# Kernel optimization log

Measured on AMD Instinct MI355X. Metric: run time of the kernel, lower is better.

## Reference

```python
import jax, jax.numpy as jnp
import numpy as np

DIM = 512
HEADS = 8
HEAD_DIM = DIM // HEADS
FF = 2048
WIN = 128
TIME_DIM = 512
B, N = 8, 8192
EPS = 1e-5
NEG = -1e9


def setup_inputs() -> dict:
    key = jax.random.key(0)
    ks = jax.random.split(key, 16)
    def lin(k, fan_in, fan_out):
        bound = 1.0 / np.sqrt(fan_in)
        kw, kb = jax.random.split(k)
        W = jax.random.uniform(kw, (fan_in, fan_out), jnp.float32, -bound, bound)
        b = jax.random.uniform(kb, (fan_out,), jnp.float32, -bound, bound)
        return W, b
    qkv_w, qkv_b = lin(ks[0], DIM, 3 * DIM)
    proj_w, proj_b = lin(ks[1], DIM, DIM)
    mlp_w1, mlp_b1 = lin(ks[2], DIM, FF)
    mlp_w2, mlp_b2 = lin(ks[3], FF, DIM)
    time_w, time_b = lin(ks[4], TIME_DIM, 2 * DIM)
    return {
        "x": jax.random.normal(ks[5], (B, N, DIM), jnp.float32),
        "t_emb": jax.random.normal(ks[6], (B, TIME_DIM), jnp.float32),
        "ln1_g": jnp.ones((DIM,), jnp.float32), "ln1_b": jnp.zeros((DIM,), jnp.float32),
        "qkv_w": qkv_w, "qkv_b": qkv_b,
        "proj_w": proj_w, "proj_b": proj_b,
        "ln2_g": jnp.ones((DIM,), jnp.float32), "ln2_b": jnp.zeros((DIM,), jnp.float32),
        "mlp_w1": mlp_w1, "mlp_b1": mlp_b1,
        "mlp_w2": mlp_w2, "mlp_b2": mlp_b2,
        "time_w": time_w, "time_b": time_b,
    }


def _layernorm(x, g, b):
    mu = jnp.mean(x, -1, keepdims=True)
    var = jnp.mean(jnp.square(x - mu), -1, keepdims=True)
    return (x - mu) * jax.lax.rsqrt(var + EPS) * g + b


def _local_attention(q, k, v, w):
    # q,k,v: [B, h, N, d]; each w-window attends to [prev|cur|next] windows.
    Bh_B, h, n, d = q.shape
    nW = n // w
    qw = q.reshape(Bh_B * h, nW, w, d)
    kw = k.reshape(Bh_B * h, nW, w, d)
    vw = v.reshape(Bh_B * h, nW, w, d)
    pad = lambda t: jnp.pad(t, ((0, 0), (1, 1), (0, 0), (0, 0)))
    kp, vp = pad(kw), pad(vw)
    # context: [Bh, nW, 3w, d]
    kc = jnp.concatenate([kp[:, :-2], kp[:, 1:-1], kp[:, 2:]], axis=2)
    vc = jnp.concatenate([vp[:, :-2], vp[:, 1:-1], vp[:, 2:]], axis=2)
    wv = jnp.pad(jnp.ones((nW,), bool), (1, 1))  # window validity
    valid = jnp.concatenate([
        jnp.repeat(wv[:-2, None], w, 1),
        jnp.repeat(wv[1:-1, None], w, 1),
        jnp.repeat(wv[2:, None], w, 1)], axis=1)  # [nW, 3w]
    sim = jnp.einsum('bnid,bnjd->bnij', qw, kc) * (d ** -0.5)
    sim = jnp.where(valid[None, :, None, :], sim, NEG)
    attn = jax.nn.softmax(sim, axis=-1)
    out = jnp.einsum('bnij,bnjd->bnid', attn, vc)
    return out.reshape(Bh_B, h, n, d)


def reference(x, t_emb, ln1_g, ln1_b, qkv_w, qkv_b, proj_w, proj_b,
              ln2_g, ln2_b, mlp_w1, mlp_b1, mlp_w2, mlp_b2, time_w, time_b):
    Bq, n, c = x.shape
    ss = jax.nn.silu(t_emb) @ time_w + time_b  # [B, 2C]
    scale, shift = ss[:, :c], ss[:, c:]
    x_norm = _layernorm(x, ln1_g, ln1_b) * (1.0 + scale[:, None, :]) + shift[:, None, :]
    qkv = (x_norm @ qkv_w + qkv_b).reshape(Bq, n, 3, HEADS, HEAD_DIM)
    qkv = jnp.transpose(qkv, (2, 0, 3, 1, 4))  # [3, B, h, N, d]
    q, k, v = qkv[0], qkv[1], qkv[2]
    attn_out = _local_attention(q, k, v, WIN)  # [B, h, N, d]
    attn_out = jnp.transpose(attn_out, (0, 2, 1, 3)).reshape(Bq, n, c)
    x = x + (attn_out @ proj_w + proj_b)
    h2 = _layernorm(x, ln2_g, ln2_b)
    mlp = jax.nn.gelu(h2 @ mlp_w1 + mlp_b1, approximate=False) @ mlp_w2 + mlp_b2
    return x + mlp
```

## Files before the change

### kernel.cpp

```cpp
#include <hip/hip_runtime.h>
#include <cstdint>
#include <cstddef>

#define DIM   512
#define HEADS 8
#define HD    64
#define FF    2048
#define WINSZ 128
#define BB    8
#define NN    8192
#define NW    (NN / WINSZ)
#define MROWS (BB * NN)
#define QS    ((size_t)BB * HEADS * NN * HD)

typedef __attribute__((ext_vector_type(8))) _Float16 half8;
typedef __attribute__((ext_vector_type(4))) float floatx4;

__device__ __forceinline__ floatx4 mfma16(half8 a, half8 b, floatx4 c) {
    return __builtin_amdgcn_mfma_f32_16x16x32_f16(a, b, c, 0, 0, 0);
}

__device__ __forceinline__ void gload_lds16(const void* g, void* l) {
    __builtin_amdgcn_global_load_lds(
        (const __attribute__((address_space(1))) void*)g,
        (__attribute__((address_space(3))) void*)l, 16, 0, 0);
}

__device__ __forceinline__ float qmax16(float v) {
    v = fmaxf(v, __shfl_xor(v, 1));
    v = fmaxf(v, __shfl_xor(v, 2));
    v = fmaxf(v, __shfl_xor(v, 4));
    v = fmaxf(v, __shfl_xor(v, 8));
    return v;
}
__device__ __forceinline__ float qsum16(float v) {
    v += __shfl_xor(v, 1);
    v += __shfl_xor(v, 2);
    v += __shfl_xor(v, 4);
    v += __shfl_xor(v, 8);
    return v;
}

__device__ __forceinline__ float gelu_f(float x) {
    const float y = 1.5957691216f * (x + 0.044715f * x * x * x);
    const float t = 1.0f - 2.0f / (__expf(y) + 1.0f);
    return 0.5f * x * (1.0f + t);
}

__global__ __launch_bounds__(128)
void time_ss_kernel(const float* __restrict__ t_emb, const float* __restrict__ tw,
                    const float* __restrict__ tb, float* __restrict__ ss) {
    __shared__ float st[512];
    const int b = blockIdx.x;
    for (int i = threadIdx.x; i < 512; i += 128) {
        float v = t_emb[b * 512 + i];
        st[i] = v / (1.0f + expf(-v));
    }
    __syncthreads();
    const int j = blockIdx.y * 128 + threadIdx.x;
    float acc = tb[j];
    for (int i = 0; i < 512; ++i) acc += st[i] * tw[i * 1024 + j];
    ss[b * 1024 + j] = acc;
}

__global__ __launch_bounds__(256)
void wcast_kernel(const float* __restrict__ w, _Float16* __restrict__ wt, int K, int N) {
    __shared__ float t[32][33];
    const int kb = blockIdx.x * 32, nb = blockIdx.y * 32;
    const int tx = threadIdx.x & 31, ty = threadIdx.x >> 5;
#pragma unroll
    for (int i = 0; i < 32; i += 8)
        t[ty + i][tx] = w[(size_t)(kb + ty + i) * N + nb + tx];
    __syncthreads();
#pragma unroll
    for (int i = 0; i < 32; i += 8)
        wt[(size_t)(nb + ty + i) * K + kb + tx] = (_Float16)t[tx][ty + i];
}

__global__ __launch_bounds__(256)
void ln_kernel(const float* __restrict__ x, const float* __restrict__ g,
               const float* __restrict__ bv, const float* __restrict__ ss,
               _Float16* __restrict__ out) {
    const int row  = blockIdx.x * 4 + (threadIdx.x >> 6);
    const int lane = threadIdx.x & 63;
    const float* xr = x + (size_t)row * DIM;
    const float4 v0 = *(const float4*)(xr + lane * 4);
    const float4 v1 = *(const float4*)(xr + 256 + lane * 4);
    float s  = v0.x + v0.y + v0.z + v0.w + v1.x + v1.y + v1.z + v1.w;
    float s2 = v0.x * v0.x + v0.y * v0.y + v0.z * v0.z + v0.w * v0.w +
               v1.x * v1.x + v1.y * v1.y + v1.z * v1.z + v1.w * v1.w;
#pragma unroll
    for (int m = 1; m < 64; m <<= 1) {
        s  += __shfl_xor(s, m);
        s2 += __shfl_xor(s2, m);
    }
    const float mean = s * (1.0f / 512.0f);
    const float var  = s2 * (1.0f / 512.0f) - mean * mean;
    const float rstd = rsqrtf(var + 1e-5f);
    const int b = row >> 13;
    const float vv[8] = {v0.x, v0.y, v0.z, v0.w, v1.x, v1.y, v1.z, v1.w};
    union { _Float16 h[4]; unsigned long long u; } pk;
#pragma unroll
    for (int half = 0; half < 2; ++half) {
        const int c0 = half * 256 + lane * 4;
#pragma unroll
        for (int i = 0; i < 4; ++i) {
            const int c = c0 + i;
            float y = (vv[half * 4 + i] - mean) * rstd * g[c] + bv[c];
            y = y * (1.0f + ss[b * 1024 + c]) + ss[b * 1024 + 512 + c];
            pk.h[i] = (_Float16)y;
        }
        *(unsigned long long*)(out + (size_t)row * DIM + c0) = pk.u;
    }
}

__global__ __launch_bounds__(256)
void ln_h_kernel(const _Float16* __restrict__ x, const float* __restrict__ g,
                 const float* __restrict__ bv, _Float16* __restrict__ out) {
    const int row  = blockIdx.x * 4 + (threadIdx.x >> 6);
    const int lane = threadIdx.x & 63;
    half8 v = *(const half8*)(x + (size_t)row * DIM + lane * 8);
    float f[8];
    float s = 0.f, s2 = 0.f;
#pragma unroll
    for (int i = 0; i < 8; ++i) {
        f[i] = (float)v[i];
        s += f[i];
        s2 += f[i] * f[i];
    }
#pragma unroll
    for (int m = 1; m < 64; m <<= 1) {
        s  += __shfl_xor(s, m);
        s2 += __shfl_xor(s2, m);
    }
    const float mean = s * (1.0f / 512.0f);
    const float var  = s2 * (1.0f / 512.0f) - mean * mean;
    const float rstd = rsqrtf(var + 1e-5f);
    half8 o;
#pragma unroll
    for (int i = 0; i < 8; ++i) {
        const int c = lane * 8 + i;
        o[i] = (_Float16)((f[i] - mean) * rstd * g[c] + bv[c]);
    }
    *(half8*)(out + (size_t)row * DIM + lane * 8) = o;
}

template <int EPI>
__global__ __launch_bounds__(256)
void gemm_bt(const _Float16* __restrict__ A, const _Float16* __restrict__ BT,
             const float* __restrict__ bias, int K, int N,
             const float* __restrict__ residf, const _Float16* __restrict__ residh,
             float* __restrict__ outf, _Float16* __restrict__ outh) {
    __shared__ _Float16 lA[128 * 64];
    __shared__ _Float16 lB[128 * 64];
    const int tid  = threadIdx.x;
    const int wv   = tid >> 6;
    const int lane = tid & 63;
    const int ln   = lane & 15;
    const int qd   = lane >> 4;
    const int wm   = (wv >> 1) * 64;
    const int wn   = (wv & 1) * 64;

    const int nbx = gridDim.x;
    const int l   = blockIdx.y * nbx + blockIdx.x;
    const int grp = l / (nbx * 8);
    const int rem = l - grp * (nbx * 8);
    const int m0  = (grp * 8 + (rem & 7)) * 128;
    const int n0  = (rem >> 3) * 128;

    floatx4 acc[4][4];
#pragma unroll
    for (int i = 0; i < 4; ++i)
#pragma unroll
        for (int j = 0; j < 4; ++j) acc[i][j] = (floatx4){0.f, 0.f, 0.f, 0.f};

    for (int kt = 0; kt < K; kt += 64) {
        __syncthreads();
#pragma unroll
        for (int i = 0; i < 4; ++i) {
            const int c   = tid + i * 256;
            const int row = c >> 3;
            const int src = ((c & 7) ^ (row & 7)) * 8;
            const int base = (wv * 64 + i * 256) * 8;
            gload_lds16(A + (size_t)(m0 + row) * K + kt + src, &lA[base]);
            gload_lds16(BT + (size_t)(n0 + row) * K + kt + src, &lB[base]);
        }
        __syncthreads();
#pragma unroll
        for (int ks = 0; ks < 2; ++ks) {
            half8 af[4], bf[4];
#pragma unroll
            for (int mi = 0; mi < 4; ++mi) {
                const int row = wm + mi * 16 + ln;
                af[mi] = *(const half8*)&lA[row * 64 + (((ks * 4 + qd) ^ (row & 7)) << 3)];
            }
#pragma unroll
            for (int ni = 0; ni < 4; ++ni) {
                const int row = wn + ni * 16 + ln;
                bf[ni] = *(const half8*)&lB[row * 64 + (((ks * 4 + qd) ^ (row & 7)) << 3)];
            }
#pragma unroll
            for (int mi = 0; mi < 4; ++mi)
#pragma unroll
                for (int ni = 0; ni < 4; ++ni)
                    acc[mi][ni] = mfma16(af[mi], bf[ni], acc[mi][ni]);
        }
    }

#pragma unroll
    for (int mi = 0; mi < 4; ++mi) {
#pragma unroll
        for (int ni = 0; ni < 4; ++ni) {
            const int col  = n0 + wn + ni * 16 + ln;
            const float bb = bias[col];
#pragma unroll
            for (int r = 0; r < 4; ++r) {
                const int row = m0 + wm + mi * 16 + qd * 4 + r;
                const float v = acc[mi][ni][r] + bb;
                if (EPI == 0) {
                    const int which = col >> 9, cc = col & 511;
                    const int b = row >> 13, t = row & 8191;
                    const int h = cc >> 6, d = cc & 63;
                    outh[(size_t)which * QS +
                         ((size_t)(b * HEADS + h) * NN + t) * HD + d] = (_Float16)v;
                } else if (EPI == 1) {
                    const size_t idx = (size_t)row * N + col;
                    outh[idx] = (_Float16)(residf[idx] + v);
                } else if (EPI == 3) {
                    const size_t idx = (size_t)row * N + col;
                    outf[idx] = (float)residh[idx] + v;
                } else {
                    outh[(size_t)row * N + col] = (_Float16)gelu_f(v);
                }
            }
        }
    }
}

__global__ __launch_bounds__(256)
void attn_kernel(const _Float16* __restrict__ qkv, _Float16* __restrict__ attn) {
    const int w  = blockIdx.x;
    const int bh = blockIdx.y;
    const int tid  = threadIdx.x;
    const int wv   = tid >> 6;
    const int lane = tid & 63;
    const int ln   = lane & 15;
    const int qd   = lane >> 4;

    __shared__ _Float16 vt[64 * 136];
    __shared__ _Float16 pl[4 * 32 * 136];

    const _Float16* qbuf = qkv;
    const _Float16* kbuf = qkv + QS;
    const _Float16* vbuf = qkv + 2 * QS;
    const size_t bhbase = (size_t)bh * NN * HD;

    half8 qf[2][2];
    const _Float16* qsrc = qbuf + bhbase + (size_t)(w * WINSZ + wv * 32) * HD;
#pragma unroll
    for (int mt = 0; mt < 2; ++mt)
#pragma unroll
        for (int ks = 0; ks < 2; ++ks)
            qf[mt][ks] = *(const half8*)(qsrc + (mt * 16 + ln) * HD + ks * 32 + qd * 8);

    float mrun[2][4], lrun[2][4];
    floatx4 oacc[2][4];
#pragma unroll
    for (int mt = 0; mt < 2; ++mt)
#pragma unroll
        for (int r = 0; r < 4; ++r) { mrun[mt][r] = -3.0e38f; lrun[mt][r] = 0.f; }
#pragma unroll
    for (int mt = 0; mt < 2; ++mt)
#pragma unroll
        for (int dt = 0; dt < 4; ++dt) oacc[mt][dt] = (floatx4){0.f, 0.f, 0.f, 0.f};

    for (int c = 0; c < 3; ++c) {
        const int kvw = w + c - 1;
        if (kvw < 0 || kvw >= NW) continue;
        __syncthreads();
        const _Float16* vsrc = vbuf + bhbase + (size_t)kvw * WINSZ * HD;
#pragma unroll
        for (int j = 0; j < 4; ++j) {
            const int cc = tid + j * 256;
            const int s = cc >> 3, d0 = (cc & 7) * 8;
            half8 vvv = *(const half8*)(vsrc + cc * 8);
#pragma unroll
            for (int e = 0; e < 8; ++e) vt[(d0 + e) * 136 + s] = vvv[e];
        }
        __syncthreads();

        const _Float16* ksrc = kbuf + bhbase + (size_t)kvw * WINSZ * HD;
        floatx4 sacc[2][8];
#pragma unroll
        for (int nt = 0; nt < 8; ++nt) {
            half8 b0 = *(const half8*)(ksrc + (nt * 16 + ln) * HD + qd * 8);
            half8 b1 = *(const half8*)(ksrc + (nt * 16 + ln) * HD + 32 + qd * 8);
#pragma unroll
            for (int mt = 0; mt < 2; ++mt) {
                floatx4 t = mfma16(qf[mt][0], b0, (floatx4){0.f, 0.f, 0.f, 0.f});
                sacc[mt][nt] = mfma16(qf[mt][1], b1, t);
            }
        }

        _Float16* pw = pl + wv * 32 * 136;
#pragma unroll
        for (int mt = 0; mt < 2; ++mt) {
#pragma unroll
            for (int r = 0; r < 4; ++r) {
                float mx = -3.0e38f;
#pragma unroll
                for (int nt = 0; nt < 8; ++nt)
                    mx = fmaxf(mx, sacc[mt][nt][r] * 0.125f);
                mx = qmax16(mx);
                const float mnew  = fmaxf(mrun[mt][r], mx);
                const float alpha = __expf(mrun[mt][r] - mnew);
                float rs = 0.f;
#pragma unroll
                for (int nt = 0; nt < 8; ++nt) {
                    const float pv = __expf(sacc[mt][nt][r] * 0.125f - mnew);
                    rs += pv;
                    pw[(mt * 16 + qd * 4 + r) * 136 + nt * 16 + ln] = (_Float16)pv;
                }
                rs = qsum16(rs);
                lrun[mt][r] = lrun[mt][r] * alpha + rs;
                mrun[mt][r] = mnew;
#pragma unroll
                for (int dt = 0; dt < 4; ++dt) oacc[mt][dt][r] *= alpha;
            }
        }

#pragma unroll
        for (int kt = 0; kt < 4; ++kt) {
            half8 pf0 = *(const half8*)(pw + ln * 136 + kt * 32 + qd * 8);
            half8 pf1 = *(const half8*)(pw + (16 + ln) * 136 + kt * 32 + qd * 8);
#pragma unroll
            for (int dt = 0; dt < 4; ++dt) {
                half8 vf = *(const half8*)&vt[(dt * 16 + ln) * 136 + kt * 32 + qd * 8];
                oacc[0][dt] = mfma16(pf0, vf, oacc[0][dt]);
                oacc[1][dt] = mfma16(pf1, vf, oacc[1][dt]);
            }
        }
    }

    const int b = bh >> 3, h = bh & 7;
#pragma unroll
    for (int mt = 0; mt < 2; ++mt) {
#pragma unroll
        for (int dt = 0; dt < 4; ++dt) {
#pragma unroll
            for (int r = 0; r < 4; ++r) {
                const int trow = w * WINSZ + wv * 32 + mt * 16 + qd * 4 + r;
                const int col  = h * HD + dt * 16 + ln;
                attn[((size_t)b * NN + trow) * DIM + col] =
                    (_Float16)(oacc[mt][dt][r] / lrun[mt][r]);
            }
        }
    }
}

extern "C" void kernel_launch(void* const* d_in, const int* in_sizes, int n_in,
                              void* d_out, int out_size, void* d_ws, size_t ws_size,
                              hipStream_t stream) {
    const float* x      = (const float*)d_in[0];
    const float* t_emb  = (const float*)d_in[1];
    const float* ln1_g  = (const float*)d_in[2];
    const float* ln1_b  = (const float*)d_in[3];
    const float* qkv_w  = (const float*)d_in[4];
    const float* qkv_b  = (const float*)d_in[5];
    const float* proj_w = (const float*)d_in[6];
    const float* proj_b = (const float*)d_in[7];
    const float* ln2_g  = (const float*)d_in[8];
    const float* ln2_b  = (const float*)d_in[9];
    const float* mlp_w1 = (const float*)d_in[10];
    const float* mlp_b1 = (const float*)d_in[11];
    const float* mlp_w2 = (const float*)d_in[12];
    const float* mlp_b2 = (const float*)d_in[13];
    const float* time_w = (const float*)d_in[14];
    const float* time_b = (const float*)d_in[15];
    float* out = (float*)d_out;

    char* p = (char*)d_ws;
    auto alloc = [&](size_t bytes) {
        char* r = p;
        p += (bytes + 255) & ~(size_t)255;
        return r;
    };
    float*    ss   = (float*)alloc(8 * 1024 * 4);
    _Float16* wq   = (_Float16*)alloc((size_t)1536 * 512 * 2);
    _Float16* wp   = (_Float16*)alloc((size_t)512 * 512 * 2);
    _Float16* w1t  = (_Float16*)alloc((size_t)2048 * 512 * 2);
    _Float16* w2t  = (_Float16*)alloc((size_t)512 * 2048 * 2);
    _Float16* h2   = (_Float16*)alloc((size_t)MROWS * 512 * 2);
    _Float16* x1h  = (_Float16*)alloc((size_t)MROWS * 512 * 2);
    _Float16* regA = (_Float16*)alloc((size_t)MROWS * 512 * 2);
    _Float16* regB = (_Float16*)alloc((size_t)3 * MROWS * 512 * 2);
    _Float16* xn     = regA;
    _Float16* attn   = regA;
    _Float16* qkvb   = regB;
    _Float16* hidden = regA;
    (void)ws_size; (void)in_sizes; (void)n_in; (void)out_size;

    wcast_kernel<<<dim3(512 / 32, 1536 / 32), 256, 0, stream>>>(qkv_w, wq, 512, 1536);
    wcast_kernel<<<dim3(512 / 32, 512 / 32), 256, 0, stream>>>(proj_w, wp, 512, 512);
    wcast_kernel<<<dim3(512 / 32, 2048 / 32), 256, 0, stream>>>(mlp_w1, w1t, 512, 2048);
    wcast_kernel<<<dim3(2048 / 32, 512 / 32), 256, 0, stream>>>(mlp_w2, w2t, 2048, 512);
    time_ss_kernel<<<dim3(8, 8), 128, 0, stream>>>(t_emb, time_w, time_b, ss);
    ln_kernel<<<dim3(MROWS / 4), 256, 0, stream>>>(x, ln1_g, ln1_b, ss, xn);
    gemm_bt<0><<<dim3(1536 / 128, MROWS / 128), 256, 0, stream>>>(
        xn, wq, qkv_b, 512, 1536, nullptr, nullptr, nullptr, qkvb);
    attn_kernel<<<dim3(NW, BB * HEADS), 256, 0, stream>>>(qkvb, attn);
    gemm_bt<1><<<dim3(512 / 128, MROWS / 128), 256, 0, stream>>>(
        attn, wp, proj_b, 512, 512, x, nullptr, nullptr, x1h);
    ln_h_kernel<<<dim3(MROWS / 4), 256, 0, stream>>>(x1h, ln2_g, ln2_b, h2);
    gemm_bt<2><<<dim3(2048 / 128, MROWS / 128), 256, 0, stream>>>(
        h2, w1t, mlp_b1, 512, 2048, nullptr, nullptr, nullptr, hidden);
    gemm_bt<3><<<dim3(512 / 128, MROWS / 128), 256, 0, stream>>>(
        hidden, w2t, mlp_b2, 2048, 512, nullptr, x1h, out, nullptr);
}
```

Before: 1.241 ms.

## Rewrite GEMM as 256x256 double-buffered LDS pipeline with 512 threads

The fp16 MFMA GEMM moves from 128x128 tiles with 256 threads and one synchronised LDS stage to 256x256 tiles with 8 waves. A double-buffered 128KB LDS ring is filled by async global_load_lds prefetches of the next K-halves, interleaved with the MFMA phases under explicit sched/s_barriers and s_setprio. The aim is to hide global-load latency behind compute and raise reuse per LDS byte. The cost is large LDS use, which limits occupancy to one block per CU despite the launch bound of 2. It also adds more accumulator registers and fewer blocks for the narrow N=512 GEMMs.

```diff
diff --git a/kernel.cpp b/kernel.cpp
--- a/kernel.cpp
+++ b/kernel.cpp
@@ -46,6 +46,10 @@
     const float t = 1.0f - 2.0f / (__expf(y) + 1.0f);
     return 0.5f * x * (1.0f + t);
 }
+
+#define SBAR() do { __builtin_amdgcn_sched_barrier(0); \
+                    __builtin_amdgcn_s_barrier();      \
+                    __builtin_amdgcn_sched_barrier(0); } while (0)
 
 __global__ __launch_bounds__(128)
 void time_ss_kernel(const float* __restrict__ t_emb, const float* __restrict__ tw,
@@ -146,77 +150,146 @@
 }
 
 template <int EPI>
-__global__ __launch_bounds__(256)
+__global__ __launch_bounds__(512, 2)
 void gemm_bt(const _Float16* __restrict__ A, const _Float16* __restrict__ BT,
              const float* __restrict__ bias, int K, int N,
              const float* __restrict__ residf, const _Float16* __restrict__ residh,
              float* __restrict__ outf, _Float16* __restrict__ outh) {
-    __shared__ _Float16 lA[128 * 64];
-    __shared__ _Float16 lB[128 * 64];
+    __shared__ __align__(16) _Float16 lds[65536];
     const int tid  = threadIdx.x;
     const int wv   = tid >> 6;
     const int lane = tid & 63;
     const int ln   = lane & 15;
     const int qd   = lane >> 4;
-    const int wm   = (wv >> 1) * 64;
-    const int wn   = (wv & 1) * 64;
+    const int wr   = wv >> 2;
+    const int wc   = wv & 3;
+    const int NT   = K >> 6;
 
     const int nbx = gridDim.x;
     const int l   = blockIdx.y * nbx + blockIdx.x;
     const int grp = l / (nbx * 8);
     const int rem = l - grp * (nbx * 8);
-    const int m0  = (grp * 8 + (rem & 7)) * 128;
-    const int n0  = (rem >> 3) * 128;
-
-    floatx4 acc[4][4];
-#pragma unroll
-    for (int i = 0; i < 4; ++i)
-#pragma unroll
-        for (int j = 0; j < 4; ++j) acc[i][j] = (floatx4){0.f, 0.f, 0.f, 0.f};
-
-    for (int kt = 0; kt < K; kt += 64) {
-        __syncthreads();
-#pragma unroll
-        for (int i = 0; i < 4; ++i) {
-            const int c   = tid + i * 256;
-            const int row = c >> 3;
-            const int src = ((c & 7) ^ (row & 7)) * 8;
-            const int base = (wv * 64 + i * 256) * 8;
-            gload_lds16(A + (size_t)(m0 + row) * K + kt + src, &lA[base]);
-            gload_lds16(BT + (size_t)(n0 + row) * K + kt + src, &lB[base]);
-        }
-        __syncthreads();
-#pragma unroll
-        for (int ks = 0; ks < 2; ++ks) {
-            half8 af[4], bf[4];
-#pragma unroll
-            for (int mi = 0; mi < 4; ++mi) {
-                const int row = wm + mi * 16 + ln;
-                af[mi] = *(const half8*)&lA[row * 64 + (((ks * 4 + qd) ^ (row & 7)) << 3)];
-            }
-#pragma unroll
-            for (int ni = 0; ni < 4; ++ni) {
-                const int row = wn + ni * 16 + ln;
-                bf[ni] = *(const half8*)&lB[row * 64 + (((ks * 4 + qd) ^ (row & 7)) << 3)];
-            }
-#pragma unroll
-            for (int mi = 0; mi < 4; ++mi)
-#pragma unroll
-                for (int ni = 0; ni < 4; ++ni)
-                    acc[mi][ni] = mfma16(af[mi], bf[ni], acc[mi][ni]);
-        }
-    }
-
-#pragma unroll
-    for (int mi = 0; mi < 4; ++mi) {
-#pragma unroll
-        for (int ni = 0; ni < 4; ++ni) {
-            const int col  = n0 + wn + ni * 16 + ln;
-            const float bb = bias[col];
+    const int m0  = (grp * 8 + (rem & 7)) * 256;
+    const int n0  = (rem >> 3) * 256;
+
+    const int c1  = tid + 512;
+    const int sr0 = tid >> 2, sr1 = c1 >> 2;
+    const int so0 = (((tid & 3) ^ (sr0 & 3)) << 3);
+    const int so1 = (((c1 & 3) ^ (sr1 & 3)) << 3);
+    const _Float16* aS0 = A  + (size_t)(m0 + sr0) * K + so0;
+    const _Float16* aS1 = A  + (size_t)(m0 + sr1) * K + so1;
+    const _Float16* bS0 = BT + (size_t)(n0 + sr0) * K + so0;
+    const _Float16* bS1 = BT + (size_t)(n0 + sr1) * K + so1;
+    const int dst0 = (wv * 64) * 8;
+    const int dst1 = (wv * 64 + 512) * 8;
+
+    auto stA = [&](int buf, int kh, int ktEl) {
+        _Float16* r = &lds[buf * 32768 + kh * 8192];
+        gload_lds16(aS0 + ktEl + kh * 32, r + dst0);
+        gload_lds16(aS1 + ktEl + kh * 32, r + dst1);
+    };
+    auto stB = [&](int buf, int kh, int ktEl) {
+        _Float16* r = &lds[buf * 32768 + 16384 + kh * 8192];
+        gload_lds16(bS0 + ktEl + kh * 32, r + dst0);
+        gload_lds16(bS1 + ktEl + kh * 32, r + dst1);
+    };
+
+    int rA[8], rB[4];
+#pragma unroll
+    for (int f = 0; f < 8; ++f) {
+        const int row = wr * 128 + f * 16 + ln;
+        rA[f] = row * 32 + ((qd ^ (row & 3)) << 3);
+    }
+#pragma unroll
+    for (int n = 0; n < 4; ++n) {
+        const int row = wc * 64 + n * 16 + ln;
+        rB[n] = row * 32 + ((qd ^ (row & 3)) << 3);
+    }
+
+    floatx4 acc[8][4];
+#pragma unroll
+    for (int f = 0; f < 8; ++f)
+#pragma unroll
+        for (int n = 0; n < 4; ++n) acc[f][n] = (floatx4){0.f, 0.f, 0.f, 0.f};
+
+    stA(0, 0, 0); stB(0, 0, 0); stA(0, 1, 0); stB(0, 1, 0);
+    stA(1, 0, 64); stB(1, 0, 64);
+    asm volatile("s_waitcnt vmcnt(4)" ::: "memory");
+    SBAR();
+
+    auto do_tile = [&](int t, int buf) {
+        const int ab = buf * 32768;
+        const int bb = buf * 32768 + 16384;
+        const bool s1 = (t + 1 < NT);
+        const bool s2 = (t + 2 < NT);
+        half8 af[4], bf[4];
+#pragma unroll
+        for (int f = 0; f < 4; ++f) af[f] = *(const half8*)&lds[ab + rA[f]];
+#pragma unroll
+        for (int n = 0; n < 4; ++n) bf[n] = *(const half8*)&lds[bb + rB[n]];
+        if (s1) stA(buf ^ 1, 1, (t + 1) * 64);
+        SBAR();
+        __builtin_amdgcn_s_setprio(1);
+#pragma unroll
+        for (int f = 0; f < 4; ++f)
+#pragma unroll
+            for (int n = 0; n < 4; ++n) acc[f][n] = mfma16(af[f], bf[n], acc[f][n]);
+        __builtin_amdgcn_s_setprio(0);
+        SBAR();
+#pragma unroll
+        for (int f = 0; f < 4; ++f) af[f] = *(const half8*)&lds[ab + rA[4 + f]];
+        if (s1) stB(buf ^ 1, 1, (t + 1) * 64);
+        SBAR();
+        __builtin_amdgcn_s_setprio(1);
+#pragma unroll
+        for (int f = 0; f < 4; ++f)
+#pragma unroll
+            for (int n = 0; n < 4; ++n) acc[4 + f][n] = mfma16(af[f], bf[n], acc[4 + f][n]);
+        __builtin_amdgcn_s_setprio(0);
+        SBAR();
+#pragma unroll
+        for (int f = 0; f < 4; ++f) af[f] = *(const half8*)&lds[ab + 8192 + rA[f]];
+#pragma unroll
+        for (int n = 0; n < 4; ++n) bf[n] = *(const half8*)&lds[bb + 8192 + rB[n]];
+        if (s2) stA(buf, 0, (t + 2) * 64);
+        SBAR();
+        __builtin_amdgcn_s_setprio(1);
+#pragma unroll
+        for (int f = 0; f < 4; ++f)
+#pragma unroll
+            for (int n = 0; n < 4; ++n) acc[f][n] = mfma16(af[f], bf[n], acc[f][n]);
+        __builtin_amdgcn_s_setprio(0);
+        SBAR();
+#pragma unroll
+        for (int f = 0; f < 4; ++f) af[f] = *(const half8*)&lds[ab + 8192 + rA[4 + f]];
+        if (s2) stB(buf, 0, (t + 2) * 64);
+        SBAR();
+        __builtin_amdgcn_s_setprio(1);
+#pragma unroll
+        for (int f = 0; f < 4; ++f)
+#pragma unroll
+            for (int n = 0; n < 4; ++n) acc[4 + f][n] = mfma16(af[f], bf[n], acc[4 + f][n]);
+        __builtin_amdgcn_s_setprio(0);
+        if (s2) asm volatile("s_waitcnt vmcnt(4)" ::: "memory");
+        else    asm volatile("s_waitcnt vmcnt(0)" ::: "memory");
+        SBAR();
+    };
+
+    for (int t = 0; t < NT; t += 2) {
+        do_tile(t, 0);
+        do_tile(t + 1, 1);
+    }
+
+#pragma unroll
+    for (int f = 0; f < 8; ++f) {
+#pragma unroll
+        for (int n = 0; n < 4; ++n) {
+            const int col  = n0 + wc * 64 + n * 16 + ln;
+            const float bbv = bias[col];
 #pragma unroll
             for (int r = 0; r < 4; ++r) {
-                const int row = m0 + wm + mi * 16 + qd * 4 + r;
-                const float v = acc[mi][ni][r] + bb;
+                const int row = m0 + wr * 128 + f * 16 + qd * 4 + r;
+                const float v = acc[f][n][r] + bbv;
                 if (EPI == 0) {
                     const int which = col >> 9, cc = col & 511;
                     const int b = row >> 13, t = row & 8191;
@@ -406,14 +479,14 @@
     wcast_kernel<<<dim3(2048 / 32, 512 / 32), 256, 0, stream>>>(mlp_w2, w2t, 2048, 512);
     time_ss_kernel<<<dim3(8, 8), 128, 0, stream>>>(t_emb, time_w, time_b, ss);
     ln_kernel<<<dim3(MROWS / 4), 256, 0, stream>>>(x, ln1_g, ln1_b, ss, xn);
-    gemm_bt<0><<<dim3(1536 / 128, MROWS / 128), 256, 0, stream>>>(
+    gemm_bt<0><<<dim3(1536 / 256, MROWS / 256), 512, 0, stream>>>(
         xn, wq, qkv_b, 512, 1536, nullptr, nullptr, nullptr, qkvb);
     attn_kernel<<<dim3(NW, BB * HEADS), 256, 0, stream>>>(qkvb, attn);
-    gemm_bt<1><<<dim3(512 / 128, MROWS / 128), 256, 0, stream>>>(
+    gemm_bt<1><<<dim3(512 / 256, MROWS / 256), 512, 0, stream>>>(
         attn, wp, proj_b, 512, 512, x, nullptr, nullptr, x1h);
     ln_h_kernel<<<dim3(MROWS / 4), 256, 0, stream>>>(x1h, ln2_g, ln2_b, h2);
-    gemm_bt<2><<<dim3(2048 / 128, MROWS / 128), 256, 0, stream>>>(
+    gemm_bt<2><<<dim3(2048 / 256, MROWS / 256), 512, 0, stream>>>(
         h2, w1t, mlp_b1, 512, 2048, nullptr, nullptr, nullptr, hidden);
-    gemm_bt<3><<<dim3(512 / 128, MROWS / 128), 256, 0, stream>>>(
+    gemm_bt<3><<<dim3(512 / 256, MROWS / 256), 512, 0, stream>>>(
         hidden, w2t, mlp_b2, 2048, 512, nullptr, x1h, out, nullptr);
 }
```

New measurement: 1.139 ms. 8.3% less time.

## Triple-buffer GEMM K-loop with 256x128 tiles and 512-thread blocks

Applied to the files above, without the earlier changes.

Restructures the shared GEMM kernel to use 256x128 output tiles computed by 8 waves, with a K step of 32 and a three-stage LDS ring buffer. Global-to-LDS loads for tile t+2 are issued before computing tile t, so there is one barrier per iteration instead of two. MFMA issue priority is raised during the compute phase. The aim is to hide global-load latency and cut barrier overhead, at the cost of larger LDS use (72 KB), which may limit how many blocks fit per CU.

```diff
diff --git a/kernel.cpp b/kernel.cpp
--- a/kernel.cpp
+++ b/kernel.cpp
@@ -46,6 +46,10 @@
     const float t = 1.0f - 2.0f / (__expf(y) + 1.0f);
     return 0.5f * x * (1.0f + t);
 }
+
+#define SBAR() do { __builtin_amdgcn_sched_barrier(0); \
+                    __builtin_amdgcn_s_barrier();      \
+                    __builtin_amdgcn_sched_barrier(0); } while (0)
 
 __global__ __launch_bounds__(128)
 void time_ss_kernel(const float* __restrict__ t_emb, const float* __restrict__ tw,
@@ -146,77 +150,101 @@
 }
 
 template <int EPI>
-__global__ __launch_bounds__(256)
+__global__ __launch_bounds__(512, 4)
 void gemm_bt(const _Float16* __restrict__ A, const _Float16* __restrict__ BT,
              const float* __restrict__ bias, int K, int N,
              const float* __restrict__ residf, const _Float16* __restrict__ residh,
              float* __restrict__ outf, _Float16* __restrict__ outh) {
-    __shared__ _Float16 lA[128 * 64];
-    __shared__ _Float16 lB[128 * 64];
+    __shared__ __align__(16) _Float16 lds[36864];
     const int tid  = threadIdx.x;
     const int wv   = tid >> 6;
     const int lane = tid & 63;
     const int ln   = lane & 15;
     const int qd   = lane >> 4;
-    const int wm   = (wv >> 1) * 64;
-    const int wn   = (wv & 1) * 64;
+    const int wr   = wv >> 1;
+    const int wc   = wv & 1;
+    const int NT   = K >> 5;
 
     const int nbx = gridDim.x;
     const int l   = blockIdx.y * nbx + blockIdx.x;
     const int grp = l / (nbx * 8);
     const int rem = l - grp * (nbx * 8);
-    const int m0  = (grp * 8 + (rem & 7)) * 128;
+    const int m0  = (grp * 8 + (rem & 7)) * 256;
     const int n0  = (rem >> 3) * 128;
 
+    const int ca0 = wv * 128 + lane;
+    const int ca1 = ca0 + 64;
+    const int cb  = wv * 64 + lane;
+    const int ra0 = ca0 >> 2, ra1 = ca1 >> 2, rb = cb >> 2;
+    const _Float16* aP0 = A + (size_t)(m0 + ra0) * K + (((ca0 & 3) ^ ((ra0 >> 1) & 3)) << 3);
+    const _Float16* aP1 = A + (size_t)(m0 + ra1) * K + (((ca1 & 3) ^ ((ra1 >> 1) & 3)) << 3);
+    const _Float16* bP  = BT + (size_t)(n0 + rb) * K + (((cb & 3) ^ ((rb >> 1) & 3)) << 3);
+    const int dA0 = wv * 1024;
+    const int dA1 = wv * 1024 + 512;
+    const int dB  = 8192 + wv * 512;
+
+    auto stage = [&](int base, int ke) {
+        gload_lds16(aP0 + ke, &lds[base + dA0]);
+        gload_lds16(aP1 + ke, &lds[base + dA1]);
+        gload_lds16(bP  + ke, &lds[base + dB]);
+    };
+
+    int rA[4], rB[4];
+#pragma unroll
+    for (int f = 0; f < 4; ++f) {
+        const int row = wr * 64 + f * 16 + ln;
+        rA[f] = row * 32 + ((qd ^ ((row >> 1) & 3)) << 3);
+    }
+#pragma unroll
+    for (int n = 0; n < 4; ++n) {
+        const int row = wc * 64 + n * 16 + ln;
+        rB[n] = 8192 + row * 32 + ((qd ^ ((row >> 1) & 3)) << 3);
+    }
+
     floatx4 acc[4][4];
 #pragma unroll
-    for (int i = 0; i < 4; ++i)
-#pragma unroll
-        for (int j = 0; j < 4; ++j) acc[i][j] = (floatx4){0.f, 0.f, 0.f, 0.f};
-
-    for (int kt = 0; kt < K; kt += 64) {
-        __syncthreads();
-#pragma unroll
-        for (int i = 0; i < 4; ++i) {
-            const int c   = tid + i * 256;
-            const int row = c >> 3;
-            const int src = ((c & 7) ^ (row & 7)) * 8;
-            const int base = (wv * 64 + i * 256) * 8;
-            gload_lds16(A + (size_t)(m0 + row) * K + kt + src, &lA[base]);
-            gload_lds16(BT + (size_t)(n0 + row) * K + kt + src, &lB[base]);
-        }
-        __syncthreads();
-#pragma unroll
-        for (int ks = 0; ks < 2; ++ks) {
-            half8 af[4], bf[4];
-#pragma unroll
-            for (int mi = 0; mi < 4; ++mi) {
-                const int row = wm + mi * 16 + ln;
-                af[mi] = *(const half8*)&lA[row * 64 + (((ks * 4 + qd) ^ (row & 7)) << 3)];
-            }
-#pragma unroll
-            for (int ni = 0; ni < 4; ++ni) {
-                const int row = wn + ni * 16 + ln;
-                bf[ni] = *(const half8*)&lB[row * 64 + (((ks * 4 + qd) ^ (row & 7)) << 3)];
-            }
-#pragma unroll
-            for (int mi = 0; mi < 4; ++mi)
-#pragma unroll
-                for (int ni = 0; ni < 4; ++ni)
-                    acc[mi][ni] = mfma16(af[mi], bf[ni], acc[mi][ni]);
-        }
-    }
-
-#pragma unroll
-    for (int mi = 0; mi < 4; ++mi) {
-#pragma unroll
-        for (int ni = 0; ni < 4; ++ni) {
-            const int col  = n0 + wn + ni * 16 + ln;
-            const float bb = bias[col];
+    for (int f = 0; f < 4; ++f)
+#pragma unroll
+        for (int n = 0; n < 4; ++n) acc[f][n] = (floatx4){0.f, 0.f, 0.f, 0.f};
+
+    stage(0, 0);
+    stage(12288, 32);
+    asm volatile("s_waitcnt vmcnt(3)" ::: "memory");
+    SBAR();
+
+    int boR = 0, boW = 24576, keW = 64;
+    for (int t = 0; t < NT; ++t) {
+        const bool more = (t + 2 < NT);
+        if (more) stage(boW, keW);
+        half8 af[4], bf[4];
+#pragma unroll
+        for (int f = 0; f < 4; ++f) af[f] = *(const half8*)&lds[boR + rA[f]];
+#pragma unroll
+        for (int n = 0; n < 4; ++n) bf[n] = *(const half8*)&lds[boR + rB[n]];
+        __builtin_amdgcn_s_setprio(1);
+#pragma unroll
+        for (int f = 0; f < 4; ++f)
+#pragma unroll
+            for (int n = 0; n < 4; ++n) acc[f][n] = mfma16(af[f], bf[n], acc[f][n]);
+        __builtin_amdgcn_s_setprio(0);
+        if (more) asm volatile("s_waitcnt vmcnt(3)" ::: "memory");
+        else      asm volatile("s_waitcnt vmcnt(0)" ::: "memory");
+        SBAR();
+        boR += 12288; if (boR == 36864) boR = 0;
+        boW += 12288; if (boW == 36864) boW = 0;
+        keW += 32;
+    }
+
+#pragma unroll
+    for (int f = 0; f < 4; ++f) {
+#pragma unroll
+        for (int n = 0; n < 4; ++n) {
+            const int col  = n0 + wc * 64 + n * 16 + ln;
+            const float bbv = bias[col];
 #pragma unroll
             for (int r = 0; r < 4; ++r) {
-                const int row = m0 + wm + mi * 16 + qd * 4 + r;
-                const float v = acc[mi][ni][r] + bb;
+                const int row = m0 + wr * 64 + f * 16 + qd * 4 + r;
+                const float v = acc[f][n][r] + bbv;
                 if (EPI == 0) {
                     const int which = col >> 9, cc = col & 511;
                     const int b = row >> 13, t = row & 8191;
@@ -406,14 +434,14 @@
     wcast_kernel<<<dim3(2048 / 32, 512 / 32), 256, 0, stream>>>(mlp_w2, w2t, 2048, 512);
     time_ss_kernel<<<dim3(8, 8), 128, 0, stream>>>(t_emb, time_w, time_b, ss);
     ln_kernel<<<dim3(MROWS / 4), 256, 0, stream>>>(x, ln1_g, ln1_b, ss, xn);
-    gemm_bt<0><<<dim3(1536 / 128, MROWS / 128), 256, 0, stream>>>(
+    gemm_bt<0><<<dim3(1536 / 128, MROWS / 256), 512, 0, stream>>>(
         xn, wq, qkv_b, 512, 1536, nullptr, nullptr, nullptr, qkvb);
     attn_kernel<<<dim3(NW, BB * HEADS), 256, 0, stream>>>(qkvb, attn);
-    gemm_bt<1><<<dim3(512 / 128, MROWS / 128), 256, 0, stream>>>(
+    gemm_bt<1><<<dim3(512 / 128, MROWS / 256), 512, 0, stream>>>(
         attn, wp, proj_b, 512, 512, x, nullptr, nullptr, x1h);
     ln_h_kernel<<<dim3(MROWS / 4), 256, 0, stream>>>(x1h, ln2_g, ln2_b, h2);
-    gemm_bt<2><<<dim3(2048 / 128, MROWS / 128), 256, 0, stream>>>(
+    gemm_bt<2><<<dim3(2048 / 128, MROWS / 256), 512, 0, stream>>>(
         h2, w1t, mlp_b1, 512, 2048, nullptr, nullptr, nullptr, hidden);
-    gemm_bt<3><<<dim3(512 / 128, MROWS / 128), 256, 0, stream>>>(
+    gemm_bt<3><<<dim3(512 / 128, MROWS / 256), 512, 0, stream>>>(
         hidden, w2t, mlp_b2, 2048, 512, nullptr, x1h, out, nullptr);
 }
```

After: 1.123 ms. 1.1x faster.
